# Kernel optimization log

Measured on AMD Instinct MI355X. Metric: run time of the kernel, lower is better.

## Reference

```python
import jax, jax.numpy as jnp
import numpy as np

B, T, D, H = 128, 2048, 512, 8
HD = D // H  # head_dim = 64

def setup_inputs() -> dict:
    key = jax.random.key(0)
    ks = jax.random.split(key, 8)
    x = jax.random.normal(ks[0], (B, T, D), dtype=jnp.float32)
    mask_bool = jax.random.randint(ks[1], (B, T), 0, 2) > 0
    temp = jnp.ones((H,), dtype=jnp.float32)
    w_sal = jax.random.normal(ks[2], (D, H), dtype=jnp.float32) * (1.0 / np.sqrt(D))
    b_sal = jnp.zeros((H,), dtype=jnp.float32)
    w_gate = jax.random.normal(ks[3], (HD, 1), dtype=jnp.float32) * (1.0 / np.sqrt(HD))
    b_gate = jnp.zeros((1,), dtype=jnp.float32)
    scale = jnp.ones((D,), dtype=jnp.float32)
    return {"x": x, "mask_bool": mask_bool, "temp": temp, "w_sal": w_sal,
            "b_sal": b_sal, "w_gate": w_gate, "b_gate": b_gate, "scale": scale}

def reference(x, mask_bool, temp, w_sal, b_sal, w_gate, b_gate, scale):
    Bx, Tx, Dx = x.shape
    x_heads = x.reshape(Bx, Tx, H, HD)
    temperature = jax.nn.softplus(temp) + 0.3              # [H]
    logits = (jnp.einsum('btd,dh->bth', x, w_sal) + b_sal) / temperature[None, None, :]
    m = mask_bool[:, :, None]                              # [B,T,1]
    safe_logits = jnp.where(m, logits, -1e9)
    max_logits = jax.lax.stop_gradient(jnp.max(safe_logits, axis=1, keepdims=True))
    exps = jnp.where(m, jnp.exp(safe_logits - max_logits), 0.0)
    weights = exps / (jnp.sum(exps, axis=1, keepdims=True) + 1e-6)  # [B,T,H]
    write_vec_heads = jnp.einsum('bth,bthd->bhd', weights, x_heads)  # [B,H,HD]
    gate_logits = jnp.einsum('bhd,do->bho', write_vec_heads, w_gate) + b_gate  # [B,H,1]
    window_valid = jnp.any(mask_bool, axis=1)[:, None, None]
    write_u_heads = jax.nn.sigmoid(gate_logits) * window_valid.astype(jnp.float32)  # [B,H,1]
    write_vec = write_vec_heads.reshape(Bx, Dx)
    rms = jnp.sqrt(jnp.mean(jnp.square(write_vec), axis=-1, keepdims=True) + 1e-6)
    write_vec = write_vec / rms * scale
    write_u_expanded = jnp.tile(write_u_heads, (1, 1, HD)).reshape(Bx, Dx)
    return (write_vec, write_u_expanded, write_u_heads.squeeze(-1))
```

## Files before the change

### kernel.cpp

```cpp
#include <hip/hip_runtime.h>

#define B_DIM 128
#define T_DIM 2048
#define D_DIM 512
#define H_DIM 8
#define HD_DIM 64
#define CH 8
#define ROWS_PER_BLOCK (T_DIM / CH)
#define ROWS_PER_WAVE (ROWS_PER_BLOCK / 4)
#define SUBS (CH * 4)

typedef float f4v __attribute__((ext_vector_type(4)));

#define ROW_BODY(ROW, B0, B1)                                                  \
  {                                                                            \
    const int row_ = (ROW);                                                    \
            \
    float p0 = B0.x * w[0];                                                    \
    float p1 = B0.x * w[1];                                                    \
    float p2 = B0.x * w[2];                                                    \
    float p3 = B0.x * w[3];                                                    \
    float p4 = B0.x * w[4];                                                    \
    float p5 = B0.x * w[5];                                                    \
    float p6 = B0.x * w[6];                                                    \
    float p7 = B0.x * w[7];                                                    \
    p0 = fmaf(B0.y, w[8+0], p0);  p1 = fmaf(B0.y, w[8+1], p1);                 \
    p2 = fmaf(B0.y, w[8+2], p2);  p3 = fmaf(B0.y, w[8+3], p3);                 \
    p4 = fmaf(B0.y, w[8+4], p4);  p5 = fmaf(B0.y, w[8+5], p5);                 \
    p6 = fmaf(B0.y, w[8+6], p6);  p7 = fmaf(B0.y, w[8+7], p7);                 \
    p0 = fmaf(B0.z, w[16+0], p0); p1 = fmaf(B0.z, w[16+1], p1);                \
    p2 = fmaf(B0.z, w[16+2], p2); p3 = fmaf(B0.z, w[16+3], p3);                \
    p4 = fmaf(B0.z, w[16+4], p4); p5 = fmaf(B0.z, w[16+5], p5);                \
    p6 = fmaf(B0.z, w[16+6], p6); p7 = fmaf(B0.z, w[16+7], p7);                \
    p0 = fmaf(B0.w, w[24+0], p0); p1 = fmaf(B0.w, w[24+1], p1);                \
    p2 = fmaf(B0.w, w[24+2], p2); p3 = fmaf(B0.w, w[24+3], p3);                \
    p4 = fmaf(B0.w, w[24+4], p4); p5 = fmaf(B0.w, w[24+5], p5);                \
    p6 = fmaf(B0.w, w[24+6], p6); p7 = fmaf(B0.w, w[24+7], p7);                \
    p0 = fmaf(B1.x, w[32+0], p0); p1 = fmaf(B1.x, w[32+1], p1);                \
    p2 = fmaf(B1.x, w[32+2], p2); p3 = fmaf(B1.x, w[32+3], p3);                \
    p4 = fmaf(B1.x, w[32+4], p4); p5 = fmaf(B1.x, w[32+5], p5);                \
    p6 = fmaf(B1.x, w[32+6], p6); p7 = fmaf(B1.x, w[32+7], p7);                \
    p0 = fmaf(B1.y, w[40+0], p0); p1 = fmaf(B1.y, w[40+1], p1);                \
    p2 = fmaf(B1.y, w[40+2], p2); p3 = fmaf(B1.y, w[40+3], p3);                \
    p4 = fmaf(B1.y, w[40+4], p4); p5 = fmaf(B1.y, w[40+5], p5);                \
    p6 = fmaf(B1.y, w[40+6], p6); p7 = fmaf(B1.y, w[40+7], p7);                \
    p0 = fmaf(B1.z, w[48+0], p0); p1 = fmaf(B1.z, w[48+1], p1);                \
    p2 = fmaf(B1.z, w[48+2], p2); p3 = fmaf(B1.z, w[48+3], p3);                \
    p4 = fmaf(B1.z, w[48+4], p4); p5 = fmaf(B1.z, w[48+5], p5);                \
    p6 = fmaf(B1.z, w[48+6], p6); p7 = fmaf(B1.z, w[48+7], p7);                \
    p0 = fmaf(B1.w, w[56+0], p0); p1 = fmaf(B1.w, w[56+1], p1);                \
    p2 = fmaf(B1.w, w[56+2], p2); p3 = fmaf(B1.w, w[56+3], p3);                \
    p4 = fmaf(B1.w, w[56+4], p4); p5 = fmaf(B1.w, w[56+5], p5);                \
    p6 = fmaf(B1.w, w[56+6], p6); p7 = fmaf(B1.w, w[56+7], p7);                \
            \
    const bool hi5 = (lane & 32) != 0;                         \
    float q0 = (hi5 ? p2 : p0) + __shfl_xor(hi5 ? p0 : p2, 32, 64);            \
    float q1 = (hi5 ? p3 : p1) + __shfl_xor(hi5 ? p1 : p3, 32, 64);            \
    float q2 = (hi5 ? p6 : p4) + __shfl_xor(hi5 ? p4 : p6, 32, 64);            \
    float q3 = (hi5 ? p7 : p5) + __shfl_xor(hi5 ? p5 : p7, 32, 64);            \
    const bool hi4 = (lane & 16) != 0;                         \
    float sA = (hi4 ? q1 : q0) + __shfl_xor(hi4 ? q0 : q1, 16, 64);            \
    float sB = (hi4 ? q3 : q2) + __shfl_xor(hi4 ? q2 : q3, 16, 64);            \
    sA += __shfl_xor(sA, 8, 64);  sB += __shfl_xor(sB, 8, 64);                 \
    sA += __shfl_xor(sA, 4, 64);  sB += __shfl_xor(sB, 4, 64);                 \
    sA += __shfl_xor(sA, 2, 64);  sB += __shfl_xor(sB, 2, 64);                 \
    sA += __shfl_xor(sA, 1, 64);  sB += __shfl_xor(sB, 1, 64);                 \
    const bool valid = (rowmask >> row_) & 1ull;                               \
    const float lgA = valid ? (sA + bsA) * invTA : -1e9f;                      \
    const float lgB = valid ? (sB + bsB) * invTB : -1e9f;                      \
    const bool needA = lgA > mA + 8.0f;                                        \
    const bool needB = lgB > mB + 8.0f;                                        \
    if (__any(needA || needB)) {                                               \
      const float mnA = needA ? lgA : mA;                                      \
      const float scA = __expf(mA - mnA);                                      \
      const float mnB = needB ? lgB : mB;                                      \
      const float scB = __expf(mB - mnB);                                      \
      lA *= scA; lB *= scB;                                                    \
      acc0 *= scA; acc1 *= scA; acc2 *= scA; acc3 *= scA;                      \
      acc4 *= scB; acc5 *= scB; acc6 *= scB; acc7 *= scB;                      \
      mA = mnA; mB = mnB;                                                      \
    }                                                                          \
    const float peA = valid ? __expf(lgA - mA) : 0.0f;                         \
    const float peB = valid ? __expf(lgB - mB) : 0.0f;                         \
    lA += peA; lB += peB;                                                      \
    acc0 = fmaf(peA, B0.x, acc0); acc1 = fmaf(peA, B0.y, acc1);                \
    acc2 = fmaf(peA, B0.z, acc2); acc3 = fmaf(peA, B0.w, acc3);                \
    acc4 = fmaf(peB, B1.x, acc4); acc5 = fmaf(peB, B1.y, acc5);                \
    acc6 = fmaf(peB, B1.z, acc6); acc7 = fmaf(peB, B1.w, acc7);                \
           \
    const int pr_ = (row_ + 2 < ROWS_PER_WAVE) ? (row_ + 2)                    \
                                               : (ROWS_PER_WAVE - 1);          \
    const f4v* pp_ = xb + (size_t)pr_ * (D_DIM / 4);                           \
    B0 = pp_[0];                                                               \
    B1 = pp_[64];                                                              \
  }

__global__ __launch_bounds__(256, 4) void salience_pass1(
    const float* __restrict__ x,
    const void* __restrict__ mask,
    const float* __restrict__ temp,
    const float* __restrict__ w_sal,
    const float* __restrict__ b_sal,
    float* __restrict__ ws_m,
    float* __restrict__ ws_l,
    float* __restrict__ ws_acc)
{
    const int b     = blockIdx.x >> 3;
    const int chunk = blockIdx.x & 7;
    const int lane  = threadIdx.x & 63;
    const int wv    = threadIdx.x >> 6;
    const int hA    = lane >> 4;

    const unsigned mv0 = (unsigned)((const int*)mask)[lane];
    const int byte_mask = (__ballot(mv0 > 1u) != 0ull) ? 1 : 0;

    float w[64];
    {
        const float4* wa = (const float4*)(w_sal) + (size_t)lane * 8;
        const float4* wb = (const float4*)(w_sal + 2048) + (size_t)lane * 8;
        #pragma unroll
        for (int q = 0; q < 8; ++q) {
            float4 v = wa[q];
            w[q*4+0] = v.x; w[q*4+1] = v.y; w[q*4+2] = v.z; w[q*4+3] = v.w;
        }
        #pragma unroll
        for (int q = 0; q < 8; ++q) {
            float4 v = wb[q];
            w[32+q*4+0] = v.x; w[32+q*4+1] = v.y; w[32+q*4+2] = v.z; w[32+q*4+3] = v.w;
        }
    }
    const float bsA = b_sal[hA];
    const float bsB = b_sal[hA + 4];
    const float tpA = temp[hA];
    const float tpB = temp[hA + 4];
    const float spA = (tpA > 20.0f) ? tpA : log1pf(__expf(tpA));
    const float spB = (tpB > 20.0f) ? tpB : log1pf(__expf(tpB));
    const float invTA = 1.0f / (spA + 0.3f);
    const float invTB = 1.0f / (spB + 0.3f);

    const int t0 = chunk * ROWS_PER_BLOCK + wv * ROWS_PER_WAVE;
    const size_t mbase = (size_t)b * T_DIM + t0;

    int mrow = byte_mask ? (int)((const unsigned char*)mask)[mbase + lane]
                         : ((const int*)mask)[mbase + lane];
    const unsigned long long rowmask = __ballot(mrow != 0);

    float mA = -1e9f, lA = 0.0f;
    float mB = -1e9f, lB = 0.0f;
    float acc0 = 0.f, acc1 = 0.f, acc2 = 0.f, acc3 = 0.f;
    float acc4 = 0.f, acc5 = 0.f, acc6 = 0.f, acc7 = 0.f;

    const f4v* xb = (const f4v*)(x + ((size_t)b * T_DIM + t0) * D_DIM) + lane;

    f4v bA0 = xb[0];
    f4v bA1 = xb[64];
    f4v bB0 = xb[128];
    f4v bB1 = xb[192];

    for (int r2 = 0; r2 < ROWS_PER_WAVE / 2; ++r2) {
        ROW_BODY(2 * r2,     bA0, bA1)
        ROW_BODY(2 * r2 + 1, bB0, bB1)
    }

    const int sub = chunk * 4 + wv;
    const size_t bc = (size_t)b * SUBS + sub;
    if ((lane & 15) == 0) {
        ws_m[bc * H_DIM + hA]     = mA;
        ws_m[bc * H_DIM + hA + 4] = mB;
        ws_l[bc * H_DIM + hA]     = lA;
        ws_l[bc * H_DIM + hA + 4] = lB;
    }
    float4* dstA = (float4*)(ws_acc + bc * D_DIM) + lane;
    dstA[0]  = make_float4(acc0, acc1, acc2, acc3);
    dstA[64] = make_float4(acc4, acc5, acc6, acc7);
}

__global__ __launch_bounds__(512) void salience_pass2(
    const float* __restrict__ ws_m,
    const float* __restrict__ ws_l,
    const float* __restrict__ ws_acc,
    const float* __restrict__ w_gate,
    const float* __restrict__ b_gate,
    const float* __restrict__ scale,
    float* __restrict__ out)
{
    const int b  = blockIdx.x;
    const int d  = threadIdx.x;
    const int h  = d >> 6;
    const int dd = d & 63;
    const int lane = d & 63;

    __shared__ float sm_e[SUBS * H_DIM];
    __shared__ float sm_L[H_DIM];
    __shared__ float red[H_DIM];

    {
        const int c = lane & 31;
        const size_t idx = ((size_t)b * SUBS + c) * H_DIM + h;
        const float mv = ws_m[idx];
        const float lv = ws_l[idx];
        float M = mv;
        M = fmaxf(M, __shfl_xor(M, 16, 64));
        M = fmaxf(M, __shfl_xor(M, 8, 64));
        M = fmaxf(M, __shfl_xor(M, 4, 64));
        M = fmaxf(M, __shfl_xor(M, 2, 64));
        M = fmaxf(M, __shfl_xor(M, 1, 64));
        const float e = __expf(mv - M);
        float Lp = lv * e;
        Lp += __shfl_xor(Lp, 16, 64);
        Lp += __shfl_xor(Lp, 8, 64);
        Lp += __shfl_xor(Lp, 4, 64);
        Lp += __shfl_xor(Lp, 2, 64);
        Lp += __shfl_xor(Lp, 1, 64);
        if (lane < 32) sm_e[c * H_DIM + h] = e;
        if (lane == 0) sm_L[h] = Lp;
    }
    __syncthreads();

    float A = 0.0f;
    const float* pa = ws_acc + (size_t)b * SUBS * D_DIM + d;
    #pragma unroll
    for (int c0 = 0; c0 < SUBS; c0 += 8) {
        float v0 = pa[(size_t)(c0+0) * D_DIM];
        float v1 = pa[(size_t)(c0+1) * D_DIM];
        float v2 = pa[(size_t)(c0+2) * D_DIM];
        float v3 = pa[(size_t)(c0+3) * D_DIM];
        float v4 = pa[(size_t)(c0+4) * D_DIM];
        float v5 = pa[(size_t)(c0+5) * D_DIM];
        float v6 = pa[(size_t)(c0+6) * D_DIM];
        float v7 = pa[(size_t)(c0+7) * D_DIM];
        A = fmaf(sm_e[(c0+0) * H_DIM + h], v0, A);
        A = fmaf(sm_e[(c0+1) * H_DIM + h], v1, A);
        A = fmaf(sm_e[(c0+2) * H_DIM + h], v2, A);
        A = fmaf(sm_e[(c0+3) * H_DIM + h], v3, A);
        A = fmaf(sm_e[(c0+4) * H_DIM + h], v4, A);
        A = fmaf(sm_e[(c0+5) * H_DIM + h], v5, A);
        A = fmaf(sm_e[(c0+6) * H_DIM + h], v6, A);
        A = fmaf(sm_e[(c0+7) * H_DIM + h], v7, A);
    }
    const float L = sm_L[h];
    const float wv = A / (L + 1e-6f);

    float g = wv * w_gate[dd];
    #pragma unroll
    for (int s = 1; s < 64; s <<= 1) g += __shfl_xor(g, s, 64);
    const float gl = g + b_gate[0];
    const float u = (L > 0.0f) ? (1.0f / (1.0f + __expf(-gl))) : 0.0f;

    float sq = wv * wv;
    #pragma unroll
    for (int s = 1; s < 64; s <<= 1) sq += __shfl_xor(sq, s, 64);
    if (dd == 0) red[h] = sq;
    __syncthreads();
    float ssum = 0.0f;
    #pragma unroll
    for (int k = 0; k < H_DIM; ++k) ssum += red[k];
    const float rms = sqrtf(ssum * (1.0f / (float)D_DIM) + 1e-6f);

    out[(size_t)b * D_DIM + d] = wv / rms * scale[d];
    out[(size_t)B_DIM * D_DIM + (size_t)b * D_DIM + d] = u;
    if (dd == 0) out[2 * (size_t)B_DIM * D_DIM + (size_t)b * H_DIM + h] = u;
}

extern "C" void kernel_launch(void* const* d_in, const int* in_sizes, int n_in,
                              void* d_out, int out_size, void* d_ws, size_t ws_size,
                              hipStream_t stream) {
    (void)in_sizes; (void)n_in; (void)out_size; (void)ws_size;
    const float* x      = (const float*)d_in[0];
    const void*  mask   = d_in[1];
    const float* temp   = (const float*)d_in[2];
    const float* w_sal  = (const float*)d_in[3];
    const float* b_sal  = (const float*)d_in[4];
    const float* w_gate = (const float*)d_in[5];
    const float* b_gate = (const float*)d_in[6];
    const float* scale  = (const float*)d_in[7];
    float* out = (float*)d_out;

    char* ws = (char*)d_ws;
    float* ws_m   = (float*)(ws + 256);
    float* ws_l   = (float*)(ws + 256 + 131072);
    float* ws_acc = (float*)(ws + 256 + 2 * 131072);

    salience_pass1<<<B_DIM * CH, 256, 0, stream>>>(
        x, mask, temp, w_sal, b_sal, ws_m, ws_l, ws_acc);
    salience_pass2<<<B_DIM, 512, 0, stream>>>(
        ws_m, ws_l, ws_acc, w_gate, b_gate, scale, out);
}
```

Measured before the change: 115.6 us.

## Stream x rows through per-wave LDS ring using async global_load_lds

Replaces the register double-buffered prefetch of x rows with a 4-deep per-wave LDS ring buffer filled by global_load_lds (direct-to-LDS) loads, synchronized with explicit vmcnt waits and sched barriers. The goal is to keep more row loads in flight per wave and hide HBM latency for this bandwidth-bound streaming reduction. It adds 32KB of LDS per block, which may limit occupancy, plus an extra LDS read per row. It also relies on vmcnt accounting being exact; the mask load, weight loads and the loop tail are sensitive to that.

```diff
diff --git a/kernel.cpp b/kernel.cpp
--- a/kernel.cpp
+++ b/kernel.cpp
@@ -9,13 +9,21 @@
 #define ROWS_PER_BLOCK (T_DIM / CH)
 #define ROWS_PER_WAVE (ROWS_PER_BLOCK / 4)
 #define SUBS (CH * 4)
+#define DEPTH 4
 
 typedef float f4v __attribute__((ext_vector_type(4)));
 
-#define ROW_BODY(ROW, B0, B1)                                                  \
+__device__ __forceinline__ void gll16(const float* g, float* l) {
+    __builtin_amdgcn_global_load_lds(
+        (const __attribute__((address_space(1))) void*)g,
+        (__attribute__((address_space(3))) void*)l, 16, 0, 0);
+}
+
+#define VMWAIT(n) asm volatile("s_waitcnt vmcnt(" #n ")" ::: "memory")
+
+#define ROW_COMPUTE(ROW, B0, B1)                                               \
   {                                                                            \
     const int row_ = (ROW);                                                    \
-            \
     float p0 = B0.x * w[0];                                                    \
     float p1 = B0.x * w[1];                                                    \
     float p2 = B0.x * w[2];                                                    \
@@ -52,7 +60,6 @@
     p2 = fmaf(B1.w, w[56+2], p2); p3 = fmaf(B1.w, w[56+3], p3);                \
     p4 = fmaf(B1.w, w[56+4], p4); p5 = fmaf(B1.w, w[56+5], p5);                \
     p6 = fmaf(B1.w, w[56+6], p6); p7 = fmaf(B1.w, w[56+7], p7);                \
-            \
     const bool hi5 = (lane & 32) != 0;                         \
     float q0 = (hi5 ? p2 : p0) + __shfl_xor(hi5 ? p0 : p2, 32, 64);            \
     float q1 = (hi5 ? p3 : p1) + __shfl_xor(hi5 ? p1 : p3, 32, 64);            \
@@ -87,12 +94,31 @@
     acc2 = fmaf(peA, B0.z, acc2); acc3 = fmaf(peA, B0.w, acc3);                \
     acc4 = fmaf(peB, B1.x, acc4); acc5 = fmaf(peB, B1.y, acc5);                \
     acc6 = fmaf(peB, B1.z, acc6); acc7 = fmaf(peB, B1.w, acc7);                \
-           \
-    const int pr_ = (row_ + 2 < ROWS_PER_WAVE) ? (row_ + 2)                    \
-                                               : (ROWS_PER_WAVE - 1);          \
-    const f4v* pp_ = xb + (size_t)pr_ * (D_DIM / 4);                           \
-    B0 = pp_[0];                                                               \
-    B1 = pp_[64];                                                              \
+  }
+
+#define BODY_MAIN(ROW)                                                         \
+  {                                                                            \
+    VMWAIT(6);                                                                 \
+    __builtin_amdgcn_sched_barrier(0);                                         \
+    const f4v* sp_ = (const f4v*)(slotp + ((ROW) & 3) * D_DIM) + lane;         \
+    f4v B0 = sp_[0];                                                           \
+    f4v B1 = sp_[64];                                                          \
+    __builtin_amdgcn_sched_barrier(0);                                         \
+    const float* g_ = xrow0 + (size_t)((ROW) + DEPTH) * D_DIM + lane * 4;      \
+    gll16(g_,       slotp + ((ROW) & 3) * D_DIM);                              \
+    gll16(g_ + 256, slotp + ((ROW) & 3) * D_DIM + 256);                        \
+    __builtin_amdgcn_sched_barrier(0);                                         \
+    ROW_COMPUTE((ROW), B0, B1)                                                 \
+  }
+
+#define BODY_TAIL(ROW, WAITN)                                                  \
+  {                                                                            \
+    VMWAIT(WAITN);                                                             \
+    __builtin_amdgcn_sched_barrier(0);                                         \
+    const f4v* sp_ = (const f4v*)(slotp + ((ROW) & 3) * D_DIM) + lane;         \
+    f4v B0 = sp_[0];                                                           \
+    f4v B1 = sp_[64];                                                          \
+    ROW_COMPUTE((ROW), B0, B1)                                                 \
   }
 
 __global__ __launch_bounds__(256, 4) void salience_pass1(
@@ -105,6 +131,8 @@
     float* __restrict__ ws_l,
     float* __restrict__ ws_acc)
 {
+    __shared__ float lds[4][DEPTH][D_DIM];
+
     const int b     = blockIdx.x >> 3;
     const int chunk = blockIdx.x & 7;
     const int lane  = threadIdx.x & 63;
@@ -113,6 +141,18 @@
 
     const unsigned mv0 = (unsigned)((const int*)mask)[lane];
     const int byte_mask = (__ballot(mv0 > 1u) != 0ull) ? 1 : 0;
+
+    const int t0 = chunk * ROWS_PER_BLOCK + wv * ROWS_PER_WAVE;
+    const float* xrow0 = x + ((size_t)b * T_DIM + t0) * D_DIM;
+    float* slotp = &lds[wv][0][0];
+
+    #pragma unroll
+    for (int s = 0; s < DEPTH; ++s) {
+        const float* g = xrow0 + (size_t)s * D_DIM + lane * 4;
+        gll16(g,       slotp + s * D_DIM);
+        gll16(g + 256, slotp + s * D_DIM + 256);
+        __builtin_amdgcn_sched_barrier(0);
+    }
 
     float w[64];
     {
@@ -138,9 +178,7 @@
     const float invTA = 1.0f / (spA + 0.3f);
     const float invTB = 1.0f / (spB + 0.3f);
 
-    const int t0 = chunk * ROWS_PER_BLOCK + wv * ROWS_PER_WAVE;
     const size_t mbase = (size_t)b * T_DIM + t0;
-
     int mrow = byte_mask ? (int)((const unsigned char*)mask)[mbase + lane]
                          : ((const int*)mask)[mbase + lane];
     const unsigned long long rowmask = __ballot(mrow != 0);
@@ -150,17 +188,14 @@
     float acc0 = 0.f, acc1 = 0.f, acc2 = 0.f, acc3 = 0.f;
     float acc4 = 0.f, acc5 = 0.f, acc6 = 0.f, acc7 = 0.f;
 
-    const f4v* xb = (const f4v*)(x + ((size_t)b * T_DIM + t0) * D_DIM) + lane;
-
-    f4v bA0 = xb[0];
-    f4v bA1 = xb[64];
-    f4v bB0 = xb[128];
-    f4v bB1 = xb[192];
-
-    for (int r2 = 0; r2 < ROWS_PER_WAVE / 2; ++r2) {
-        ROW_BODY(2 * r2,     bA0, bA1)
-        ROW_BODY(2 * r2 + 1, bB0, bB1)
-    }
+    #pragma unroll 4
+    for (int r = 0; r < ROWS_PER_WAVE - DEPTH; ++r) {
+        BODY_MAIN(r)
+    }
+    BODY_TAIL(ROWS_PER_WAVE - 4, 6)
+    BODY_TAIL(ROWS_PER_WAVE - 3, 4)
+    BODY_TAIL(ROWS_PER_WAVE - 2, 2)
+    BODY_TAIL(ROWS_PER_WAVE - 1, 0)
 
     const int sub = chunk * 4 + wv;
     const size_t bc = (size_t)b * SUBS + sub;
```

Result: slower. 119.3 us (+3.2%).

## Merge per-wave softmax partials in shared memory before writing workspace

Applied to the files above, without the earlier changes.

Pass 1 now uses 512-thread blocks (8 waves) over 4 chunks per batch instead of 256-thread blocks over 8 chunks. Each block combines its waves' online-softmax partials in LDS and writes one merged partial per chunk. Pass 2 then reads only 4 partials per batch instead of 32, which cuts workspace writes and reads. In exchange pass 1 gains a block-wide barrier and an LDS reduction, and has half as many blocks, which may lower occupancy given the 64-register weight array.

```diff
diff --git a/kernel.cpp b/kernel.cpp
--- a/kernel.cpp
+++ b/kernel.cpp
@@ -5,17 +5,16 @@
 #define D_DIM 512
 #define H_DIM 8
 #define HD_DIM 64
-#define CH 8
+#define CH 4
 #define ROWS_PER_BLOCK (T_DIM / CH)
-#define ROWS_PER_WAVE (ROWS_PER_BLOCK / 4)
-#define SUBS (CH * 4)
+#define WAVES 8
+#define ROWS_PER_WAVE (ROWS_PER_BLOCK / WAVES)
 
 typedef float f4v __attribute__((ext_vector_type(4)));
 
 #define ROW_BODY(ROW, B0, B1)                                                  \
   {                                                                            \
     const int row_ = (ROW);                                                    \
-            \
     float p0 = B0.x * w[0];                                                    \
     float p1 = B0.x * w[1];                                                    \
     float p2 = B0.x * w[2];                                                    \
@@ -52,7 +51,6 @@
     p2 = fmaf(B1.w, w[56+2], p2); p3 = fmaf(B1.w, w[56+3], p3);                \
     p4 = fmaf(B1.w, w[56+4], p4); p5 = fmaf(B1.w, w[56+5], p5);                \
     p6 = fmaf(B1.w, w[56+6], p6); p7 = fmaf(B1.w, w[56+7], p7);                \
-            \
     const bool hi5 = (lane & 32) != 0;                         \
     float q0 = (hi5 ? p2 : p0) + __shfl_xor(hi5 ? p0 : p2, 32, 64);            \
     float q1 = (hi5 ? p3 : p1) + __shfl_xor(hi5 ? p1 : p3, 32, 64);            \
@@ -87,7 +85,6 @@
     acc2 = fmaf(peA, B0.z, acc2); acc3 = fmaf(peA, B0.w, acc3);                \
     acc4 = fmaf(peB, B1.x, acc4); acc5 = fmaf(peB, B1.y, acc5);                \
     acc6 = fmaf(peB, B1.z, acc6); acc7 = fmaf(peB, B1.w, acc7);                \
-           \
     const int pr_ = (row_ + 2 < ROWS_PER_WAVE) ? (row_ + 2)                    \
                                                : (ROWS_PER_WAVE - 1);          \
     const f4v* pp_ = xb + (size_t)pr_ * (D_DIM / 4);                           \
@@ -95,18 +92,22 @@
     B1 = pp_[64];                                                              \
   }
 
-__global__ __launch_bounds__(256, 4) void salience_pass1(
+__global__ __launch_bounds__(512, 4) void salience_pass1(
     const float* __restrict__ x,
     const void* __restrict__ mask,
     const float* __restrict__ temp,
     const float* __restrict__ w_sal,
     const float* __restrict__ b_sal,
-    float* __restrict__ ws_m,
-    float* __restrict__ ws_l,
-    float* __restrict__ ws_acc)
+    float* __restrict__ ws_hm,
+    float* __restrict__ ws_hl,
+    float* __restrict__ ws_hacc)
 {
-    const int b     = blockIdx.x >> 3;
-    const int chunk = blockIdx.x & 7;
+    __shared__ float sm_acc[WAVES][D_DIM];
+    __shared__ float sm_m[WAVES][H_DIM];
+    __shared__ float sm_l[WAVES][H_DIM];
+
+    const int b     = blockIdx.x >> 2;
+    const int chunk = blockIdx.x & 3;
     const int lane  = threadIdx.x & 63;
     const int wv    = threadIdx.x >> 6;
     const int hA    = lane >> 4;
@@ -162,23 +163,41 @@
         ROW_BODY(2 * r2 + 1, bB0, bB1)
     }
 
-    const int sub = chunk * 4 + wv;
-    const size_t bc = (size_t)b * SUBS + sub;
     if ((lane & 15) == 0) {
-        ws_m[bc * H_DIM + hA]     = mA;
-        ws_m[bc * H_DIM + hA + 4] = mB;
-        ws_l[bc * H_DIM + hA]     = lA;
-        ws_l[bc * H_DIM + hA + 4] = lB;
-    }
-    float4* dstA = (float4*)(ws_acc + bc * D_DIM) + lane;
+        sm_m[wv][hA]     = mA;
+        sm_m[wv][hA + 4] = mB;
+        sm_l[wv][hA]     = lA;
+        sm_l[wv][hA + 4] = lB;
+    }
+    float4* dstA = (float4*)(&sm_acc[wv][0]) + lane;
     dstA[0]  = make_float4(acc0, acc1, acc2, acc3);
     dstA[64] = make_float4(acc4, acc5, acc6, acc7);
+    __syncthreads();
+
+    const int d = threadIdx.x;
+    const int h = d >> 6;
+    float M = -3.0e38f;
+    #pragma unroll
+    for (int s = 0; s < WAVES; ++s) M = fmaxf(M, sm_m[s][h]);
+    float A = 0.0f, L = 0.0f;
+    #pragma unroll
+    for (int s = 0; s < WAVES; ++s) {
+        const float e = __expf(sm_m[s][h] - M);
+        L = fmaf(sm_l[s][h], e, L);
+        A = fmaf(sm_acc[s][d], e, A);
+    }
+    const size_t hc = (size_t)b * CH + chunk;
+    ws_hacc[hc * D_DIM + d] = A;
+    if ((d & 63) == 0) {
+        ws_hm[hc * H_DIM + h] = M;
+        ws_hl[hc * H_DIM + h] = L;
+    }
 }
 
 __global__ __launch_bounds__(512) void salience_pass2(
-    const float* __restrict__ ws_m,
-    const float* __restrict__ ws_l,
-    const float* __restrict__ ws_acc,
+    const float* __restrict__ ws_hm,
+    const float* __restrict__ ws_hl,
+    const float* __restrict__ ws_hacc,
     const float* __restrict__ w_gate,
     const float* __restrict__ b_gate,
     const float* __restrict__ scale,
@@ -188,57 +207,27 @@
     const int d  = threadIdx.x;
     const int h  = d >> 6;
     const int dd = d & 63;
-    const int lane = d & 63;
-
-    __shared__ float sm_e[SUBS * H_DIM];
-    __shared__ float sm_L[H_DIM];
+
     __shared__ float red[H_DIM];
 
-    {
-        const int c = lane & 31;
-        const size_t idx = ((size_t)b * SUBS + c) * H_DIM + h;
-        const float mv = ws_m[idx];
-        const float lv = ws_l[idx];
-        float M = mv;
-        M = fmaxf(M, __shfl_xor(M, 16, 64));
-        M = fmaxf(M, __shfl_xor(M, 8, 64));
-        M = fmaxf(M, __shfl_xor(M, 4, 64));
-        M = fmaxf(M, __shfl_xor(M, 2, 64));
-        M = fmaxf(M, __shfl_xor(M, 1, 64));
-        const float e = __expf(mv - M);
-        float Lp = lv * e;
-        Lp += __shfl_xor(Lp, 16, 64);
-        Lp += __shfl_xor(Lp, 8, 64);
-        Lp += __shfl_xor(Lp, 4, 64);
-        Lp += __shfl_xor(Lp, 2, 64);
-        Lp += __shfl_xor(Lp, 1, 64);
-        if (lane < 32) sm_e[c * H_DIM + h] = e;
-        if (lane == 0) sm_L[h] = Lp;
-    }
-    __syncthreads();
-
-    float A = 0.0f;
-    const float* pa = ws_acc + (size_t)b * SUBS * D_DIM + d;
-    #pragma unroll
-    for (int c0 = 0; c0 < SUBS; c0 += 8) {
-        float v0 = pa[(size_t)(c0+0) * D_DIM];
-        float v1 = pa[(size_t)(c0+1) * D_DIM];
-        float v2 = pa[(size_t)(c0+2) * D_DIM];
-        float v3 = pa[(size_t)(c0+3) * D_DIM];
-        float v4 = pa[(size_t)(c0+4) * D_DIM];
-        float v5 = pa[(size_t)(c0+5) * D_DIM];
-        float v6 = pa[(size_t)(c0+6) * D_DIM];
-        float v7 = pa[(size_t)(c0+7) * D_DIM];
-        A = fmaf(sm_e[(c0+0) * H_DIM + h], v0, A);
-        A = fmaf(sm_e[(c0+1) * H_DIM + h], v1, A);
-        A = fmaf(sm_e[(c0+2) * H_DIM + h], v2, A);
-        A = fmaf(sm_e[(c0+3) * H_DIM + h], v3, A);
-        A = fmaf(sm_e[(c0+4) * H_DIM + h], v4, A);
-        A = fmaf(sm_e[(c0+5) * H_DIM + h], v5, A);
-        A = fmaf(sm_e[(c0+6) * H_DIM + h], v6, A);
-        A = fmaf(sm_e[(c0+7) * H_DIM + h], v7, A);
-    }
-    const float L = sm_L[h];
+    const size_t h0 = (size_t)b * CH;
+    const float m0 = ws_hm[(h0 + 0) * H_DIM + h];
+    const float m1 = ws_hm[(h0 + 1) * H_DIM + h];
+    const float m2 = ws_hm[(h0 + 2) * H_DIM + h];
+    const float m3 = ws_hm[(h0 + 3) * H_DIM + h];
+    const float M  = fmaxf(fmaxf(m0, m1), fmaxf(m2, m3));
+    const float e0 = __expf(m0 - M);
+    const float e1 = __expf(m1 - M);
+    const float e2 = __expf(m2 - M);
+    const float e3 = __expf(m3 - M);
+    const float L = ws_hl[(h0 + 0) * H_DIM + h] * e0
+                  + ws_hl[(h0 + 1) * H_DIM + h] * e1
+                  + ws_hl[(h0 + 2) * H_DIM + h] * e2
+                  + ws_hl[(h0 + 3) * H_DIM + h] * e3;
+    const float A = ws_hacc[(h0 + 0) * D_DIM + d] * e0
+                  + ws_hacc[(h0 + 1) * D_DIM + d] * e1
+                  + ws_hacc[(h0 + 2) * D_DIM + d] * e2
+                  + ws_hacc[(h0 + 3) * D_DIM + d] * e3;
     const float wv = A / (L + 1e-6f);
 
     float g = wv * w_gate[dd];
@@ -277,12 +266,12 @@
     float* out = (float*)d_out;
 
     char* ws = (char*)d_ws;
-    float* ws_m   = (float*)(ws + 256);
-    float* ws_l   = (float*)(ws + 256 + 131072);
-    float* ws_acc = (float*)(ws + 256 + 2 * 131072);
-
-    salience_pass1<<<B_DIM * CH, 256, 0, stream>>>(
-        x, mask, temp, w_sal, b_sal, ws_m, ws_l, ws_acc);
+    float* ws_hm   = (float*)(ws);
+    float* ws_hl   = (float*)(ws + 16384);
+    float* ws_hacc = (float*)(ws + 32768);
+
+    salience_pass1<<<B_DIM * CH, WAVES * 64, 0, stream>>>(
+        x, mask, temp, w_sal, b_sal, ws_hm, ws_hl, ws_hacc);
     salience_pass2<<<B_DIM, 512, 0, stream>>>(
-        ws_m, ws_l, ws_acc, w_gate, b_gate, scale, out);
+        ws_hm, ws_hl, ws_hacc, w_gate, b_gate, scale, out);
 }
```

Measured after the change: 113.2 us, median of 2. 1.02x faster.
